# Optimization experiments

Measured on AMD Instinct MI355X. Metric: run time of the kernel, lower is better.

The kernel has to match this reference:

```python
import jax, jax.numpy as jnp
import numpy as np

D_MODEL = 768
N_HEADS = 12
D_K = D_MODEL // N_HEADS


def setup_inputs() -> dict:
    key = jax.random.key(0)
    ks = jax.random.split(key, 9)
    B, S = 4, 2048
    sc = 1.0 / np.sqrt(D_MODEL)
    inp = {"x": jax.random.normal(ks[0], (B, S, D_MODEL), dtype=jnp.float32)}
    names = ["q", "k", "v", "o"]
    for i, n in enumerate(names):
        inp[f"W{n}"] = jax.random.normal(ks[1 + 2 * i], (D_MODEL, D_MODEL), dtype=jnp.float32) * sc
        inp[f"b{n}"] = jax.random.normal(ks[2 + 2 * i], (D_MODEL,), dtype=jnp.float32) * 0.01
    return inp


def reference(x, Wq, bq, Wk, bk, Wv, bv, Wo, bo):
    B, S, _ = x.shape
    def split_heads(t):  # [B,S,D] -> [B,H,S,d_k]
        return t.reshape(B, S, N_HEADS, D_K).transpose(0, 2, 1, 3)
    Q = split_heads(x @ Wq.T + bq)
    K = split_heads(x @ Wk.T + bk)
    V = split_heads(x @ Wv.T + bv)
    # NOTE: original divides by d_k, not sqrt(d_k)
    scores = jnp.einsum("bhqd,bhkd->bhqk", Q, K) / D_K
    scores = jax.nn.softmax(scores, axis=-1)
    att = jnp.einsum("bhqk,bhkd->bhqd", scores, V)  # [B,H,S,d_k]
    att = att.transpose(0, 2, 1, 3).reshape(B, S, D_MODEL)
    return att @ Wo.T + bo
```

## Files before the change

kernel.cpp:

```cpp
#include <hip/hip_runtime.h>
#include <hip/hip_bf16.h>

typedef __bf16 bf16;
typedef _Float16 f16;
typedef bf16 bf16x8 __attribute__((ext_vector_type(8)));
typedef bf16 bf16x4 __attribute__((ext_vector_type(4)));
typedef f16 f16x4 __attribute__((ext_vector_type(4)));
typedef float f32x4 __attribute__((ext_vector_type(4)));

#define SLEN 2048
#define HEADS 12
#define DMODEL 768
#define MROWS 8192

#define GLOAD16(g, l) \
    __builtin_amdgcn_global_load_lds((const __attribute__((address_space(1))) void*)(g), \
                                     (__attribute__((address_space(3))) void*)(l), 16, 0, 0)

__global__ void cvt_kernel(const float* __restrict__ src, bf16* __restrict__ dst, int n4) {
    int idx = blockIdx.x * blockDim.x + threadIdx.x;
    if (idx < n4) {
        float4 v = ((const float4*)src)[idx];
        bf16x4 o;
        o[0] = (bf16)v.x; o[1] = (bf16)v.y; o[2] = (bf16)v.z; o[3] = (bf16)v.w;
        *(bf16x4*)(dst + (size_t)idx * 4) = o;
    }
}

__global__ __launch_bounds__(256, 3) void gemm_qkv(
    const bf16* __restrict__ A, const bf16* __restrict__ Bw,
    const float* __restrict__ bq, const float* __restrict__ bk, const float* __restrict__ bv,
    bf16* __restrict__ Qb, bf16* __restrict__ Kb, f16* __restrict__ VTb)
{
    __shared__ bf16 As[128][32];
    __shared__ bf16 Bs[128][32];
    const int K = DMODEL;
    int tid = threadIdx.x;
    int w = tid >> 6, lane = tid & 63, i16 = lane & 15, q4 = lane >> 4;
    int mblk = (w & 1) * 64, nblk = (w >> 1) * 64;
    int row0 = blockIdx.y * 128, col0 = blockIdx.x * 128;
    int srow = (lane >> 2), scol = (lane & 3) * 8;
    f32x4 acc[4][4] = {};

    for (int k0 = 0; k0 < K; k0 += 32) {
        __syncthreads();
        GLOAD16(A  + (size_t)(row0 + w * 16 +      srow) * K + k0 + scol, &As[w * 16][0]);
        GLOAD16(A  + (size_t)(row0 + w * 16 + 64 + srow) * K + k0 + scol, &As[w * 16 + 64][0]);
        GLOAD16(Bw + (size_t)(col0 + w * 16 +      srow) * K + k0 + scol, &Bs[w * 16][0]);
        GLOAD16(Bw + (size_t)(col0 + w * 16 + 64 + srow) * K + k0 + scol, &Bs[w * 16 + 64][0]);
        __syncthreads();
        bf16x8 af[4], bfr[4];
#pragma unroll
        for (int t = 0; t < 4; ++t) af[t] = *(const bf16x8*)(&As[mblk + t * 16 + i16][q4 * 8]);
#pragma unroll
        for (int t = 0; t < 4; ++t) bfr[t] = *(const bf16x8*)(&Bs[nblk + t * 16 + i16][q4 * 8]);
#pragma unroll
        for (int mt = 0; mt < 4; ++mt)
#pragma unroll
            for (int nt = 0; nt < 4; ++nt)
                acc[mt][nt] = __builtin_amdgcn_mfma_f32_16x16x32_bf16(af[mt], bfr[nt], acc[mt][nt], 0, 0, 0);
    }

    int region = col0 / DMODEL;
#pragma unroll
    for (int mt = 0; mt < 4; ++mt) {
        int srow_base = row0 + mblk + mt * 16 + q4 * 4;
#pragma unroll
        for (int nt = 0; nt < 4; ++nt) {
            int sc_ = col0 + nblk + nt * 16 + i16;
            int c = sc_ - region * DMODEL;
            int h = c >> 6, d = c & 63;
#pragma unroll
            for (int r = 0; r < 4; ++r) {
                int rr = srow_base + r;
                int b = rr >> 11, s = rr & 2047;
                float v = acc[mt][nt][r];
                if (region == 0) {
                    v = (v + bq[c]) * 0.0225421217f;
                    Qb[(((size_t)(b * HEADS + h)) * SLEN + s) * 64 + d] = (bf16)v;
                } else if (region == 1) {
                    v = v + bk[c];
                    Kb[(((size_t)(b * HEADS + h)) * SLEN + s) * 64 + d] = (bf16)v;
                } else {
                    v = v + bv[c];
                    VTb[(((size_t)(b * HEADS + h)) * 64 + d) * SLEN + s] = (f16)v;
                }
            }
        }
    }
}

__global__ __launch_bounds__(256, 3) void gemm_out(
    const bf16* __restrict__ A, const bf16* __restrict__ Bw,
    const float* __restrict__ bo, float* __restrict__ out)
{
    __shared__ bf16 As[128][32];
    __shared__ bf16 Bs[128][32];
    const int K = DMODEL;
    int tid = threadIdx.x;
    int w = tid >> 6, lane = tid & 63, i16 = lane & 15, q4 = lane >> 4;
    int mblk = (w & 1) * 64, nblk = (w >> 1) * 64;
    int row0 = blockIdx.y * 128, col0 = blockIdx.x * 128;
    int srow = (lane >> 2), scol = (lane & 3) * 8;
    f32x4 acc[4][4] = {};

    for (int k0 = 0; k0 < K; k0 += 32) {
        __syncthreads();
        GLOAD16(A  + (size_t)(row0 + w * 16 +      srow) * K + k0 + scol, &As[w * 16][0]);
        GLOAD16(A  + (size_t)(row0 + w * 16 + 64 + srow) * K + k0 + scol, &As[w * 16 + 64][0]);
        GLOAD16(Bw + (size_t)(col0 + w * 16 +      srow) * K + k0 + scol, &Bs[w * 16][0]);
        GLOAD16(Bw + (size_t)(col0 + w * 16 + 64 + srow) * K + k0 + scol, &Bs[w * 16 + 64][0]);
        __syncthreads();
        bf16x8 af[4], bfr[4];
#pragma unroll
        for (int t = 0; t < 4; ++t) af[t] = *(const bf16x8*)(&As[mblk + t * 16 + i16][q4 * 8]);
#pragma unroll
        for (int t = 0; t < 4; ++t) bfr[t] = *(const bf16x8*)(&Bs[nblk + t * 16 + i16][q4 * 8]);
#pragma unroll
        for (int mt = 0; mt < 4; ++mt)
#pragma unroll
            for (int nt = 0; nt < 4; ++nt)
                acc[mt][nt] = __builtin_amdgcn_mfma_f32_16x16x32_bf16(af[mt], bfr[nt], acc[mt][nt], 0, 0, 0);
    }

#pragma unroll
    for (int mt = 0; mt < 4; ++mt) {
        int srow_base = row0 + mblk + mt * 16 + q4 * 4;
#pragma unroll
        for (int nt = 0; nt < 4; ++nt) {
            int sc_ = col0 + nblk + nt * 16 + i16;
            float bb = bo[sc_];
#pragma unroll
            for (int r = 0; r < 4; ++r)
                out[(size_t)(srow_base + r) * DMODEL + sc_] = acc[mt][nt][r] + bb;
        }
    }
}

__global__ __launch_bounds__(256, 4) void attn_kernel(
    const bf16* __restrict__ Qb, const bf16* __restrict__ Kb,
    const f16* __restrict__ VTb, bf16* __restrict__ att)
{
    __shared__ bf16 Ks[128][72];
    __shared__ f16  Vt[64][136];

    int tid = threadIdx.x;
    int w = tid >> 6, lane = tid & 63, i16 = lane & 15, q4 = lane >> 4;
    int qt = blockIdx.x, h = blockIdx.y, b = blockIdx.z;
    size_t bh = (size_t)b * HEADS + h;
    const bf16* Qp = Qb + (bh * SLEN + qt * 128 + w * 32) * 64;
    const bf16* Kp = Kb + bh * SLEN * 64;
    const f16*  Vp = VTb + bh * 64 * SLEN;

    bf16x8 aq[2][2];
#pragma unroll
    for (int qs = 0; qs < 2; ++qs) {
        aq[qs][0] = *(const bf16x8*)(Qp + (qs * 16 + i16) * 64 + q4 * 8);
        aq[qs][1] = *(const bf16x8*)(Qp + (qs * 16 + i16) * 64 + 32 + q4 * 8);
    }

    f32x4 oacc[2][4] = {};
    float lsum[2] = {0.f, 0.f};

    for (int kt = 0; kt < 16; ++kt) {
        int k0 = kt * 128;
        __syncthreads();
#pragma unroll
        for (int it = 0; it < 4; ++it) {
            int cidx = it * 256 + tid;
            int key = cidx >> 3, c8 = cidx & 7;
            *(uint4*)(&Ks[key][c8 * 8]) = *(const uint4*)(Kp + (size_t)(k0 + key) * 64 + c8 * 8);
            int d = cidx >> 4, c16 = cidx & 15;
            *(uint4*)(&Vt[d][c16 * 8]) = *(const uint4*)(Vp + (size_t)d * SLEN + k0 + c16 * 8);
        }
        __syncthreads();

        f16x4 pf[2][8];
#pragma unroll
        for (int t = 0; t < 8; ++t) {
            bf16x8 kf0 = *(const bf16x8*)(&Ks[t * 16 + i16][q4 * 8]);
            bf16x8 kf1 = *(const bf16x8*)(&Ks[t * 16 + i16][32 + q4 * 8]);
#pragma unroll
            for (int qs = 0; qs < 2; ++qs) {
                f32x4 z = {};
                z = __builtin_amdgcn_mfma_f32_16x16x32_bf16(kf0, aq[qs][0], z, 0, 0, 0);
                z = __builtin_amdgcn_mfma_f32_16x16x32_bf16(kf1, aq[qs][1], z, 0, 0, 0);
                f16x4 p;
#pragma unroll
                for (int r = 0; r < 4; ++r) {
                    float e = __builtin_amdgcn_exp2f(z[r]);
                    lsum[qs] += e;
                    p[r] = (f16)e;
                }
                pf[qs][t] = p;
            }
        }

#pragma unroll
        for (int t = 0; t < 8; ++t) {
#pragma unroll
            for (int dt = 0; dt < 4; ++dt) {
                f16x4 vf = *(const f16x4*)(&Vt[dt * 16 + i16][t * 16 + q4 * 4]);
                oacc[0][dt] = __builtin_amdgcn_mfma_f32_16x16x16f16(vf, pf[0][t], oacc[0][dt], 0, 0, 0);
                oacc[1][dt] = __builtin_amdgcn_mfma_f32_16x16x16f16(vf, pf[1][t], oacc[1][dt], 0, 0, 0);
            }
        }
    }

#pragma unroll
    for (int qs = 0; qs < 2; ++qs) {
        float l = lsum[qs];
        l += __shfl_xor(l, 16);
        l += __shfl_xor(l, 32);
        float inv = 1.f / l;
        int row = qt * 128 + w * 32 + qs * 16 + i16;
        size_t obase = ((size_t)b * SLEN + row) * DMODEL + h * 64;
#pragma unroll
        for (int dt = 0; dt < 4; ++dt) {
            bf16x4 o;
#pragma unroll
            for (int r = 0; r < 4; ++r) o[r] = (bf16)(oacc[qs][dt][r] * inv);
            *(bf16x4*)(att + obase + dt * 16 + q4 * 4) = o;
        }
    }
}

extern "C" void kernel_launch(void* const* d_in, const int* in_sizes, int n_in,
                              void* d_out, int out_size, void* d_ws, size_t ws_size,
                              hipStream_t stream) {
    const float* x  = (const float*)d_in[0];
    const float* Wq = (const float*)d_in[1];
    const float* bq = (const float*)d_in[2];
    const float* Wk = (const float*)d_in[3];
    const float* bk = (const float*)d_in[4];
    const float* Wv = (const float*)d_in[5];
    const float* bv = (const float*)d_in[6];
    const float* Wo = (const float*)d_in[7];
    const float* bo = (const float*)d_in[8];
    float* out = (float*)d_out;

    char* ws = (char*)d_ws;
    bf16* xb   = (bf16*)(ws);
    bf16* wqkv = (bf16*)(ws + 12582912);
    bf16* wob  = (bf16*)(ws + 16121856);
    bf16* Qb   = (bf16*)(ws + 17301504);
    bf16* Kb   = (bf16*)(ws + 29884416);
    f16*  VTb  = (f16*)(ws + 42467328);
    bf16* attb = xb;

    cvt_kernel<<<6144, 256, 0, stream>>>(x, xb, 1572864);
    cvt_kernel<<<576, 256, 0, stream>>>(Wq, wqkv, 147456);
    cvt_kernel<<<576, 256, 0, stream>>>(Wk, wqkv + 589824, 147456);
    cvt_kernel<<<576, 256, 0, stream>>>(Wv, wqkv + 1179648, 147456);
    cvt_kernel<<<576, 256, 0, stream>>>(Wo, wob, 147456);

    gemm_qkv<<<dim3(18, 64), 256, 0, stream>>>(xb, wqkv, bq, bk, bv, Qb, Kb, VTb);
    attn_kernel<<<dim3(16, 12, 4), 256, 0, stream>>>(Qb, Kb, VTb, attb);
    gemm_out<<<dim3(6, 64), 256, 0, stream>>>(attb, wob, bo, out);
}
```

Before: 274.5 us.

## Double-buffer GEMM tiles, prefetch attention K/V via registers, merge weight conversions

Both GEMMs now double-buffer their LDS tiles, so the next k-slice's async global-to-LDS loads are issued before the current slice's MFMAs, with one barrier per iteration instead of two. The attention kernel prefetches the next K/V tile into registers while computing on the current one, and interleaves the P·V MFMAs per key subtile instead of buffering all P fragments. The V epilogue writes four consecutive sequence positions as one vector store. The four weight conversion launches are merged into one 2D launch. The aim is to hide global load latency and cut launch overhead, at the cost of more LDS in the GEMMs and more registers in attention, which may reduce occupancy.

```diff
diff --git a/kernel.cpp b/kernel.cpp
--- a/kernel.cpp
+++ b/kernel.cpp
@@ -27,13 +27,33 @@
     }
 }
 
+__global__ void cvt4_kernel(const float* __restrict__ s0, const float* __restrict__ s1,
+                            const float* __restrict__ s2, const float* __restrict__ s3,
+                            bf16* __restrict__ d0, bf16* __restrict__ d1,
+                            bf16* __restrict__ d2, bf16* __restrict__ d3, int n4) {
+    const float* s; bf16* d;
+    switch (blockIdx.y) {
+        case 0: s = s0; d = d0; break;
+        case 1: s = s1; d = d1; break;
+        case 2: s = s2; d = d2; break;
+        default: s = s3; d = d3; break;
+    }
+    int idx = blockIdx.x * blockDim.x + threadIdx.x;
+    if (idx < n4) {
+        float4 v = ((const float4*)s)[idx];
+        bf16x4 o;
+        o[0] = (bf16)v.x; o[1] = (bf16)v.y; o[2] = (bf16)v.z; o[3] = (bf16)v.w;
+        *(bf16x4*)(d + (size_t)idx * 4) = o;
+    }
+}
+
 __global__ __launch_bounds__(256, 3) void gemm_qkv(
     const bf16* __restrict__ A, const bf16* __restrict__ Bw,
     const float* __restrict__ bq, const float* __restrict__ bk, const float* __restrict__ bv,
     bf16* __restrict__ Qb, bf16* __restrict__ Kb, f16* __restrict__ VTb)
 {
-    __shared__ bf16 As[128][32];
-    __shared__ bf16 Bs[128][32];
+    __shared__ bf16 As[2][128][32];
+    __shared__ bf16 Bs[2][128][32];
     const int K = DMODEL;
     int tid = threadIdx.x;
     int w = tid >> 6, lane = tid & 63, i16 = lane & 15, q4 = lane >> 4;
@@ -42,49 +62,60 @@
     int srow = (lane >> 2), scol = (lane & 3) * 8;
     f32x4 acc[4][4] = {};
 
-    for (int k0 = 0; k0 < K; k0 += 32) {
-        __syncthreads();
-        GLOAD16(A  + (size_t)(row0 + w * 16 +      srow) * K + k0 + scol, &As[w * 16][0]);
-        GLOAD16(A  + (size_t)(row0 + w * 16 + 64 + srow) * K + k0 + scol, &As[w * 16 + 64][0]);
-        GLOAD16(Bw + (size_t)(col0 + w * 16 +      srow) * K + k0 + scol, &Bs[w * 16][0]);
-        GLOAD16(Bw + (size_t)(col0 + w * 16 + 64 + srow) * K + k0 + scol, &Bs[w * 16 + 64][0]);
-        __syncthreads();
+    const bf16* Ab = A  + (size_t)(row0 + w * 16 + srow) * K + scol;
+    const bf16* Bb = Bw + (size_t)(col0 + w * 16 + srow) * K + scol;
+
+#define STAGE(buf, k0) do { \
+        GLOAD16(Ab + (k0),              &As[buf][w * 16][0]); \
+        GLOAD16(Ab + (size_t)64 * K + (k0), &As[buf][w * 16 + 64][0]); \
+        GLOAD16(Bb + (k0),              &Bs[buf][w * 16][0]); \
+        GLOAD16(Bb + (size_t)64 * K + (k0), &Bs[buf][w * 16 + 64][0]); \
+    } while (0)
+
+    STAGE(0, 0);
+    __syncthreads();
+    int buf = 0;
+    for (int k0 = 0; k0 < K; k0 += 32, buf ^= 1) {
+        if (k0 + 32 < K) STAGE(buf ^ 1, k0 + 32);
         bf16x8 af[4], bfr[4];
 #pragma unroll
-        for (int t = 0; t < 4; ++t) af[t] = *(const bf16x8*)(&As[mblk + t * 16 + i16][q4 * 8]);
-#pragma unroll
-        for (int t = 0; t < 4; ++t) bfr[t] = *(const bf16x8*)(&Bs[nblk + t * 16 + i16][q4 * 8]);
+        for (int t = 0; t < 4; ++t) af[t] = *(const bf16x8*)(&As[buf][mblk + t * 16 + i16][q4 * 8]);
+#pragma unroll
+        for (int t = 0; t < 4; ++t) bfr[t] = *(const bf16x8*)(&Bs[buf][nblk + t * 16 + i16][q4 * 8]);
 #pragma unroll
         for (int mt = 0; mt < 4; ++mt)
 #pragma unroll
             for (int nt = 0; nt < 4; ++nt)
                 acc[mt][nt] = __builtin_amdgcn_mfma_f32_16x16x32_bf16(af[mt], bfr[nt], acc[mt][nt], 0, 0, 0);
-    }
+        __syncthreads();
+    }
+#undef STAGE
 
     int region = col0 / DMODEL;
 #pragma unroll
     for (int mt = 0; mt < 4; ++mt) {
         int srow_base = row0 + mblk + mt * 16 + q4 * 4;
+        int b = srow_base >> 11, s = srow_base & 2047;
 #pragma unroll
         for (int nt = 0; nt < 4; ++nt) {
             int sc_ = col0 + nblk + nt * 16 + i16;
             int c = sc_ - region * DMODEL;
             int h = c >> 6, d = c & 63;
-#pragma unroll
-            for (int r = 0; r < 4; ++r) {
-                int rr = srow_base + r;
-                int b = rr >> 11, s = rr & 2047;
-                float v = acc[mt][nt][r];
-                if (region == 0) {
-                    v = (v + bq[c]) * 0.0225421217f;
-                    Qb[(((size_t)(b * HEADS + h)) * SLEN + s) * 64 + d] = (bf16)v;
-                } else if (region == 1) {
-                    v = v + bk[c];
-                    Kb[(((size_t)(b * HEADS + h)) * SLEN + s) * 64 + d] = (bf16)v;
-                } else {
-                    v = v + bv[c];
-                    VTb[(((size_t)(b * HEADS + h)) * 64 + d) * SLEN + s] = (f16)v;
+            if (region == 2) {
+                f16x4 vv;
+#pragma unroll
+                for (int r = 0; r < 4; ++r) vv[r] = (f16)(acc[mt][nt][r] + bv[c]);
+                *(f16x4*)(&VTb[((size_t)(b * HEADS + h) * 64 + d) * SLEN + s]) = vv;
+            } else if (region == 0) {
+#pragma unroll
+                for (int r = 0; r < 4; ++r) {
+                    float v = (acc[mt][nt][r] + bq[c]) * 0.0225421217f;
+                    Qb[(((size_t)(b * HEADS + h)) * SLEN + s + r) * 64 + d] = (bf16)v;
                 }
+            } else {
+#pragma unroll
+                for (int r = 0; r < 4; ++r)
+                    Kb[(((size_t)(b * HEADS + h)) * SLEN + s + r) * 64 + d] = (bf16)(acc[mt][nt][r] + bk[c]);
             }
         }
     }
@@ -94,8 +125,8 @@
     const bf16* __restrict__ A, const bf16* __restrict__ Bw,
     const float* __restrict__ bo, float* __restrict__ out)
 {
-    __shared__ bf16 As[128][32];
-    __shared__ bf16 Bs[128][32];
+    __shared__ bf16 As[2][128][32];
+    __shared__ bf16 Bs[2][128][32];
     const int K = DMODEL;
     int tid = threadIdx.x;
     int w = tid >> 6, lane = tid & 63, i16 = lane & 15, q4 = lane >> 4;
@@ -104,24 +135,34 @@
     int srow = (lane >> 2), scol = (lane & 3) * 8;
     f32x4 acc[4][4] = {};
 
-    for (int k0 = 0; k0 < K; k0 += 32) {
-        __syncthreads();
-        GLOAD16(A  + (size_t)(row0 + w * 16 +      srow) * K + k0 + scol, &As[w * 16][0]);
-        GLOAD16(A  + (size_t)(row0 + w * 16 + 64 + srow) * K + k0 + scol, &As[w * 16 + 64][0]);
-        GLOAD16(Bw + (size_t)(col0 + w * 16 +      srow) * K + k0 + scol, &Bs[w * 16][0]);
-        GLOAD16(Bw + (size_t)(col0 + w * 16 + 64 + srow) * K + k0 + scol, &Bs[w * 16 + 64][0]);
-        __syncthreads();
+    const bf16* Ab = A  + (size_t)(row0 + w * 16 + srow) * K + scol;
+    const bf16* Bb = Bw + (size_t)(col0 + w * 16 + srow) * K + scol;
+
+#define STAGE(buf, k0) do { \
+        GLOAD16(Ab + (k0),              &As[buf][w * 16][0]); \
+        GLOAD16(Ab + (size_t)64 * K + (k0), &As[buf][w * 16 + 64][0]); \
+        GLOAD16(Bb + (k0),              &Bs[buf][w * 16][0]); \
+        GLOAD16(Bb + (size_t)64 * K + (k0), &Bs[buf][w * 16 + 64][0]); \
+    } while (0)
+
+    STAGE(0, 0);
+    __syncthreads();
+    int buf = 0;
+    for (int k0 = 0; k0 < K; k0 += 32, buf ^= 1) {
+        if (k0 + 32 < K) STAGE(buf ^ 1, k0 + 32);
         bf16x8 af[4], bfr[4];
 #pragma unroll
-        for (int t = 0; t < 4; ++t) af[t] = *(const bf16x8*)(&As[mblk + t * 16 + i16][q4 * 8]);
-#pragma unroll
-        for (int t = 0; t < 4; ++t) bfr[t] = *(const bf16x8*)(&Bs[nblk + t * 16 + i16][q4 * 8]);
+        for (int t = 0; t < 4; ++t) af[t] = *(const bf16x8*)(&As[buf][mblk + t * 16 + i16][q4 * 8]);
+#pragma unroll
+        for (int t = 0; t < 4; ++t) bfr[t] = *(const bf16x8*)(&Bs[buf][nblk + t * 16 + i16][q4 * 8]);
 #pragma unroll
         for (int mt = 0; mt < 4; ++mt)
 #pragma unroll
             for (int nt = 0; nt < 4; ++nt)
                 acc[mt][nt] = __builtin_amdgcn_mfma_f32_16x16x32_bf16(af[mt], bfr[nt], acc[mt][nt], 0, 0, 0);
-    }
+        __syncthreads();
+    }
+#undef STAGE
 
 #pragma unroll
     for (int mt = 0; mt < 4; ++mt) {
@@ -161,49 +202,67 @@
 
     f32x4 oacc[2][4] = {};
     float lsum[2] = {0.f, 0.f};
+    uint4 kreg[4], vreg[4];
+
+#pragma unroll
+    for (int it = 0; it < 4; ++it) {
+        int cidx = it * 256 + tid;
+        kreg[it] = *(const uint4*)(Kp + (size_t)(cidx >> 3) * 64 + (cidx & 7) * 8);
+        vreg[it] = *(const uint4*)(Vp + (size_t)(cidx >> 4) * SLEN + (cidx & 15) * 8);
+    }
+#pragma unroll
+    for (int it = 0; it < 4; ++it) {
+        int cidx = it * 256 + tid;
+        *(uint4*)(&Ks[cidx >> 3][(cidx & 7) * 8]) = kreg[it];
+        *(uint4*)(&Vt[cidx >> 4][(cidx & 15) * 8]) = vreg[it];
+    }
+    __syncthreads();
 
     for (int kt = 0; kt < 16; ++kt) {
-        int k0 = kt * 128;
-        __syncthreads();
-#pragma unroll
-        for (int it = 0; it < 4; ++it) {
-            int cidx = it * 256 + tid;
-            int key = cidx >> 3, c8 = cidx & 7;
-            *(uint4*)(&Ks[key][c8 * 8]) = *(const uint4*)(Kp + (size_t)(k0 + key) * 64 + c8 * 8);
-            int d = cidx >> 4, c16 = cidx & 15;
-            *(uint4*)(&Vt[d][c16 * 8]) = *(const uint4*)(Vp + (size_t)d * SLEN + k0 + c16 * 8);
-        }
-        __syncthreads();
-
-        f16x4 pf[2][8];
+        if (kt < 15) {
+            int k0 = (kt + 1) * 128;
+#pragma unroll
+            for (int it = 0; it < 4; ++it) {
+                int cidx = it * 256 + tid;
+                kreg[it] = *(const uint4*)(Kp + (size_t)(k0 + (cidx >> 3)) * 64 + (cidx & 7) * 8);
+                vreg[it] = *(const uint4*)(Vp + (size_t)(cidx >> 4) * SLEN + k0 + (cidx & 15) * 8);
+            }
+        }
+
 #pragma unroll
         for (int t = 0; t < 8; ++t) {
             bf16x8 kf0 = *(const bf16x8*)(&Ks[t * 16 + i16][q4 * 8]);
             bf16x8 kf1 = *(const bf16x8*)(&Ks[t * 16 + i16][32 + q4 * 8]);
+            f16x4 p[2];
 #pragma unroll
             for (int qs = 0; qs < 2; ++qs) {
                 f32x4 z = {};
                 z = __builtin_amdgcn_mfma_f32_16x16x32_bf16(kf0, aq[qs][0], z, 0, 0, 0);
                 z = __builtin_amdgcn_mfma_f32_16x16x32_bf16(kf1, aq[qs][1], z, 0, 0, 0);
-                f16x4 p;
 #pragma unroll
                 for (int r = 0; r < 4; ++r) {
                     float e = __builtin_amdgcn_exp2f(z[r]);
                     lsum[qs] += e;
-                    p[r] = (f16)e;
+                    p[qs][r] = (f16)e;
                 }
-                pf[qs][t] = p;
-            }
-        }
-
-#pragma unroll
-        for (int t = 0; t < 8; ++t) {
+            }
 #pragma unroll
             for (int dt = 0; dt < 4; ++dt) {
                 f16x4 vf = *(const f16x4*)(&Vt[dt * 16 + i16][t * 16 + q4 * 4]);
-                oacc[0][dt] = __builtin_amdgcn_mfma_f32_16x16x16f16(vf, pf[0][t], oacc[0][dt], 0, 0, 0);
-                oacc[1][dt] = __builtin_amdgcn_mfma_f32_16x16x16f16(vf, pf[1][t], oacc[1][dt], 0, 0, 0);
-            }
+                oacc[0][dt] = __builtin_amdgcn_mfma_f32_16x16x16f16(vf, p[0], oacc[0][dt], 0, 0, 0);
+                oacc[1][dt] = __builtin_amdgcn_mfma_f32_16x16x16f16(vf, p[1], oacc[1][dt], 0, 0, 0);
+            }
+        }
+
+        __syncthreads();
+        if (kt < 15) {
+#pragma unroll
+            for (int it = 0; it < 4; ++it) {
+                int cidx = it * 256 + tid;
+                *(uint4*)(&Ks[cidx >> 3][(cidx & 7) * 8]) = kreg[it];
+                *(uint4*)(&Vt[cidx >> 4][(cidx & 15) * 8]) = vreg[it];
+            }
+            __syncthreads();
         }
     }
 
@@ -249,10 +308,8 @@
     bf16* attb = xb;
 
     cvt_kernel<<<6144, 256, 0, stream>>>(x, xb, 1572864);
-    cvt_kernel<<<576, 256, 0, stream>>>(Wq, wqkv, 147456);
-    cvt_kernel<<<576, 256, 0, stream>>>(Wk, wqkv + 589824, 147456);
-    cvt_kernel<<<576, 256, 0, stream>>>(Wv, wqkv + 1179648, 147456);
-    cvt_kernel<<<576, 256, 0, stream>>>(Wo, wob, 147456);
+    cvt4_kernel<<<dim3(576, 4), 256, 0, stream>>>(Wq, Wk, Wv, Wo,
+                                                  wqkv, wqkv + 589824, wqkv + 1179648, wob, 147456);
 
     gemm_qkv<<<dim3(18, 64), 256, 0, stream>>>(xb, wqkv, bq, bk, bv, Qb, Kb, VTb);
     attn_kernel<<<dim3(16, 12, 4), 256, 0, stream>>>(Qb, Kb, VTb, attb);
```

Measured after the change: 408.8 us. +48.9%, slower.
